# Performance work log

Measured on AMD Instinct MI355X. Metric: run time of the kernel, lower is better.

Reference implementation:

```python
import jax, jax.numpy as jnp
import numpy as np

B, T, C, E = 2, 100, 80, 32
MH = MW = 64
IN_H = IN_W = 640.0
IOU_FACTOR, CLS_FACTOR, TOPK = 6.0, 0.5, 10
EPS = 1e-9


def get_anchors_and_scalers(fmaps, in_h, in_w):
    anchors, scalers = [], []
    for fh, fw in fmaps:
        stride = in_h / fh
        ys = (np.arange(fh) + 0.5) * stride
        xs = (np.arange(fw) + 0.5) * stride
        gy, gx = np.meshgrid(ys, xs, indexing='ij')
        anchors.append(np.stack([gx, gy], -1).reshape(-1, 2))
        scalers.append(np.full(fh * fw, stride))
    return (np.concatenate(anchors).astype(np.float32),
            np.concatenate(scalers).astype(np.float32))


def setup_inputs() -> dict:
    key = jax.random.key(0)
    ks = jax.random.split(key, 8)
    anchors_np, scalers_np = get_anchors_and_scalers([(80, 80), (40, 40), (20, 20)], IN_H, IN_W)
    anchors = jnp.asarray(anchors_np)
    scalers = jnp.asarray(scalers_np)
    A = anchors.shape[0]
    cls_logits = jax.random.normal(ks[0], (B, A, C), jnp.float32)
    wh = jax.random.uniform(ks[1], (B, A, 2), jnp.float32, 16.0, 160.0)
    ctr = anchors[None] + jax.random.normal(ks[2], (B, A, 2), jnp.float32) * 8.0
    pred_boxes = jnp.clip(jnp.concatenate([ctr - wh / 2, ctr + wh / 2], -1), 0.0, IN_W)
    mask_embs = jax.random.normal(ks[3], (B, A, E), jnp.float32)
    protos = jax.random.normal(ks[4], (B, MH, MW, E), jnp.float32)
    tl = jax.random.uniform(ks[5], (B, T, 2), jnp.float32, 0.0, 560.0)
    twh = jax.random.uniform(ks[6], (B, T, 2), jnp.float32, 30.0, 240.0)
    target_bbox = jnp.concatenate([tl, jnp.minimum(tl + twh, IN_W)], -1)
    target_cls = jax.random.randint(ks[7], (B, T), 0, C, jnp.int32)
    target_masks = (jax.random.uniform(jax.random.fold_in(key, 7), (B, MH, MW, T)) > 0.5).astype(jnp.float32)
    return {'cls_logits': cls_logits, 'pred_boxes': pred_boxes, 'mask_embs': mask_embs,
            'protos': protos, 'target_cls': target_cls, 'target_bbox': target_bbox,
            'target_masks': target_masks, 'anchors': anchors, 'scalers': scalers}


def _ciou_pairwise(gt, pr):
    # gt [B,T,4], pr [B,A,4] -> [B,T,A]
    g = gt[:, :, None, :]
    p = pr[:, None, :, :]
    ix1 = jnp.maximum(g[..., 0], p[..., 0]); iy1 = jnp.maximum(g[..., 1], p[..., 1])
    ix2 = jnp.minimum(g[..., 2], p[..., 2]); iy2 = jnp.minimum(g[..., 3], p[..., 3])
    inter = jnp.clip(ix2 - ix1, 0.0) * jnp.clip(iy2 - iy1, 0.0)
    wg = g[..., 2] - g[..., 0]; hg = g[..., 3] - g[..., 1]
    wp = p[..., 2] - p[..., 0]; hp = p[..., 3] - p[..., 1]
    union = wg * hg + wp * hp - inter + EPS
    iou = inter / union
    cw = jnp.maximum(g[..., 2], p[..., 2]) - jnp.minimum(g[..., 0], p[..., 0])
    ch = jnp.maximum(g[..., 3], p[..., 3]) - jnp.minimum(g[..., 1], p[..., 1])
    c2 = cw * cw + ch * ch + EPS
    rho2 = ((g[..., 0] + g[..., 2] - p[..., 0] - p[..., 2]) ** 2 +
            (g[..., 1] + g[..., 3] - p[..., 1] - p[..., 3]) ** 2) / 4.0
    v = (4.0 / (jnp.pi ** 2)) * (jnp.arctan(wg / (hg + EPS)) - jnp.arctan(wp / (hp + EPS))) ** 2
    alpha = jax.lax.stop_gradient(v / (1.0 - iou + v + EPS))
    return iou - rho2 / c2 - alpha * v


def _bbox_mask(boxes, mh, mw, in_h, in_w):
    # boxes [B,A,4] pixel xyxy -> [B,A,mh,mw] binary inside-box mask on mask grid
    sx, sy = mw / in_w, mh / in_h
    x1, y1, x2, y2 = boxes[..., 0] * sx, boxes[..., 1] * sy, boxes[..., 2] * sx, boxes[..., 3] * sy
    rows = jnp.arange(mh, dtype=boxes.dtype)
    cols = jnp.arange(mw, dtype=boxes.dtype)
    rm = (rows >= y1[..., None]) & (rows < y2[..., None])  # [B,A,mh]
    cm = (cols >= x1[..., None]) & (cols < x2[..., None])  # [B,A,mw]
    return (rm[..., :, None] & cm[..., None, :]).astype(boxes.dtype)


def _assign_and_build(cls_logits, pred_boxes, mask_embs, protos,
                      target_cls, target_bbox, target_masks, anchors, scalers):
    Bn, A, Cn = cls_logits.shape
    mh, mw = protos.shape[1], protos.shape[2]
    # --- task-aligned assigner ---
    lt, rb = target_bbox[:, :, None, :2], target_bbox[:, :, None, 2:]
    deltas = jnp.concatenate([anchors[None, None] - lt, rb - anchors[None, None]], -1)
    grid_mask = (jnp.min(deltas, -1) > 0).astype(cls_logits.dtype)  # [B,T,A]
    iou_mat = jnp.clip(_ciou_pairwise(target_bbox, pred_boxes), 0.0, 1.0)  # [B,T,A]
    cls_prob = jax.nn.sigmoid(cls_logits)  # [B,A,C]
    oh_t = jax.nn.one_hot(target_cls, Cn, dtype=cls_prob.dtype)  # [B,T,C]
    cls_mat = jnp.einsum('btc,bac->bta', oh_t, cls_prob)  # [B,T,A]
    tmat = grid_mask * (iou_mat ** IOU_FACTOR) * (cls_mat ** CLS_FACTOR)
    kth = jax.lax.top_k(tmat, TOPK)[0][..., -1:]  # [B,T,1]
    topk_targets = jnp.where((tmat >= kth) & (tmat > 0), tmat, 0.0)
    unique_idx = jnp.argmax(topk_targets, axis=1)  # [B,A] best GT per anchor
    valid = (jnp.sum(topk_targets, axis=1) > 0).astype(cls_logits.dtype)  # [B,A]
    align_bbox = jnp.take_along_axis(target_bbox, jnp.broadcast_to(unique_idx[..., None], (Bn, A, 4)), axis=1)
    align_cls_idx = jnp.take_along_axis(target_cls, unique_idx, axis=1)  # [B,A]
    max_target = jnp.max(tmat, axis=-1, keepdims=True)
    max_iou = jnp.max(iou_mat, axis=-1, keepdims=True)
    norm_term = tmat / (max_target + EPS) * max_iou  # [B,T,A]
    norm_g = jnp.take_along_axis(jnp.transpose(norm_term, (0, 2, 1)), unique_idx[..., None], axis=2)  # [B,A,1]
    align_cls = jax.nn.one_hot(align_cls_idx, Cn, dtype=cls_logits.dtype) * norm_g * valid[..., None]
    # --- loss-target assembly (compute_loss body) ---
    align_bbox_scaled = align_bbox / scalers[None, :, None]
    boxes_scaled = pred_boxes / scalers[None, :, None]
    box_target = jnp.concatenate([align_bbox_scaled, valid[..., None], align_cls], -1)
    box_mask = _bbox_mask(align_bbox, mh, mw, IN_H, IN_W)  # [B,A,mh,mw]
    valid_seg = box_mask * valid[..., None, None]
    seg_pred = jax.nn.sigmoid(jnp.einsum('bne,bhwe->bnhw', mask_embs, protos)) * valid_seg
    seg_pred = seg_pred.reshape(Bn, A, mh * mw)
    masks_t = jnp.transpose(target_masks, (0, 3, 1, 2))  # [B,T,mh,mw]
    idx4 = jnp.broadcast_to(unique_idx[..., None, None], (Bn, A, mh, mw))
    align_seg = (jnp.take_along_axis(masks_t, idx4, axis=1) * valid_seg).reshape(Bn, A, mh * mw)
    area = ((align_bbox[..., 2] - align_bbox[..., 0]) * (align_bbox[..., 3] - align_bbox[..., 1])
            / (IN_W * IN_H))
    seg_target = jnp.concatenate([area[..., None], valid[..., None], align_seg], -1)
    return jnp.concatenate([boxes_scaled, cls_logits, box_target, seg_pred, seg_target], -1)


def reference(cls_logits, pred_boxes, mask_embs, protos, target_cls, target_bbox,
              target_masks, anchors, scalers):
    return _assign_and_build(cls_logits, pred_boxes, mask_embs, protos,
                             target_cls, target_bbox, target_masks, anchors, scalers)
```

## Files before the change

### kernel.cpp

```cpp
#include <hip/hip_runtime.h>
#include <math.h>

#define A_TOT 8400
#define B_N   2
#define T_N   100
#define C_N   80
#define E_N   32
#define MH_N  64
#define MW_N  64
#define ROW_N 8363
#define NROWS (B_N*A_TOT)
#define EPSF  1e-9f
#define PARAM_STRIDE 12
#define COMP_CAP 1536

typedef float vfloat4 __attribute__((ext_vector_type(4)));

__device__ __forceinline__ float2 tmat_eval(
    float gx1, float gy1, float gx2, float gy2,
    float ax,  float ay,
    float px1, float py1, float px2, float py2,
    float cl) {
  float ix1 = fmaxf(gx1,px1), iy1 = fmaxf(gy1,py1);
  float ix2 = fminf(gx2,px2), iy2 = fminf(gy2,py2);
  float inter = fmaxf(ix2-ix1,0.f) * fmaxf(iy2-iy1,0.f);
  float wg = gx2-gx1, hg = gy2-gy1, wp = px2-px1, hp = py2-py1;
  float uni = wg*hg + wp*hp - inter + EPSF;
  float iou = inter / uni;
  float cw = fmaxf(gx2,px2) - fminf(gx1,px1);
  float ch = fmaxf(gy2,py2) - fminf(gy1,py1);
  float c2 = cw*cw + ch*ch + EPSF;
  float dx = gx1+gx2-px1-px2, dy = gy1+gy2-py1-py2;
  float rho2 = (dx*dx + dy*dy) * 0.25f;
  float da = atanf(wg/(hg+EPSF)) - atanf(wp/(hp+EPSF));
  float v  = 0.4052847345693511f * da * da;
  float alpha = v / (1.f - iou + v + EPSF);
  float ciou = iou - rho2/c2 - alpha*v;
  float iouc = fminf(fmaxf(ciou, 0.f), 1.f);

  float tm = 0.f;
  if (ax > gx1 && ay > gy1 && ax < gx2 && ay < gy2) {
    float cp = 1.f / (1.f + expf(-cl));
    float i2 = iouc * iouc;
    tm = i2*i2*i2 * sqrtf(cp);
  }
  return make_float2(tm, iouc);
}

__global__ __launch_bounds__(256) void k_score(
    const float* __restrict__ cls_logits, const float* __restrict__ pred_boxes,
    const float* __restrict__ target_bbox, const int* __restrict__ target_cls,
    const float* __restrict__ anchors,
    float* __restrict__ tmat,
    float* __restrict__ kth, float* __restrict__ maxt, float* __restrict__ maxiou) {
  int bt  = blockIdx.x;
  int b   = bt / T_N;
  int tid = threadIdx.x;
  __shared__ float comp[COMP_CAP];
  __shared__ float red[256];
  __shared__ int   cnt, sidx;
  if (tid == 0) cnt = 0;
  __syncthreads();

  float4 g = *(const float4*)(target_bbox + bt*4);
  int   tc = target_cls[bt];
  float* trow = tmat + (size_t)bt * A_TOT;

  float lm = 0.f, li = 0.f;
  for (int a = tid; a < A_TOT; a += 256) {
    float ax = anchors[a*2+0], ay = anchors[a*2+1];
    float4 pb = *(const float4*)(pred_boxes + ((size_t)(b*A_TOT+a))*4);
    float cl = cls_logits[((size_t)(b*A_TOT+a))*C_N + tc];
    float2 r = tmat_eval(g.x,g.y,g.z,g.w, ax,ay, pb.x,pb.y,pb.z,pb.w, cl);
    trow[a] = r.x;
    li = fmaxf(li, r.y);
    if (r.x > 0.f) {
      lm = fmaxf(lm, r.x);
      int i = atomicAdd(&cnt, 1);
      if (i < COMP_CAP) comp[i] = r.x;
    }
  }
  red[tid] = lm; __syncthreads();
  for (int s = 128; s > 0; s >>= 1) { if (tid < s) red[tid] = fmaxf(red[tid], red[tid+s]); __syncthreads(); }
  if (tid == 0) maxt[bt] = red[0];
  __syncthreads();
  red[tid] = li; __syncthreads();
  for (int s = 128; s > 0; s >>= 1) { if (tid < s) red[tid] = fmaxf(red[tid], red[tid+s]); __syncthreads(); }
  if (tid == 0) maxiou[bt] = red[0];
  __syncthreads();
  int count = min(cnt, COMP_CAP);

  float cur = -1e30f;
  for (int k = 0; k < 10; k++) {
    float l = -1e30f;
    for (int i = tid; i < count; i += 256) l = fmaxf(l, comp[i]);
    red[tid] = l; __syncthreads();
    for (int s = 128; s > 0; s >>= 1) { if (tid < s) red[tid] = fmaxf(red[tid], red[tid+s]); __syncthreads(); }
    float m = red[0];
    if (tid == 0) sidx = 0x7fffffff;
    __syncthreads();
    if (m > -1e30f) {
      for (int i = tid; i < count; i += 256) if (comp[i] == m) atomicMin(&sidx, i);
    }
    __syncthreads();
    if (tid == 0 && sidx != 0x7fffffff) comp[sidx] = -1e30f;
    cur = m;
    __syncthreads();
  }
  if (tid == 0) kth[bt] = fmaxf(cur, 0.f);
}

__global__ __launch_bounds__(64) void k_assign(
    const float* __restrict__ tmat,
    const float* __restrict__ kth, const float* __restrict__ maxt, const float* __restrict__ maxiou,
    const float* __restrict__ target_bbox, const int* __restrict__ target_cls,
    const float* __restrict__ scalers,
    float* __restrict__ params) {
  int b   = blockIdx.y;
  int tid = threadIdx.x;
  int a   = blockIdx.x * 64 + tid;
  __shared__ float kths[T_N];
  for (int i = tid; i < T_N; i += 64) kths[i] = kth[b*T_N + i];
  __syncthreads();
  if (a >= A_TOT) return;

  const float* col = tmat + (size_t)b * T_N * A_TOT + a;
  float best = 0.f; int u = 0, any = 0;
  #pragma unroll 4
  for (int t = 0; t < T_N; t++) {
    float v = col[(size_t)t * A_TOT];
    if (v > 0.f && v >= kths[t]) {
      any = 1;
      if (v > best) { best = v; u = t; }
    }
  }
  int bu = b*T_N + u;
  float ng = any ? best / (maxt[bu] + EPSF) * maxiou[bu] : 0.f;
  float4 tb = *(const float4*)(target_bbox + bu*4);
  float s = scalers[a];
  float area = (tb.z - tb.x) * (tb.w - tb.y) / (640.f*640.f);

  int row = b*A_TOT + a;
  float* pp = params + (size_t)row * PARAM_STRIDE;
  *(float4*)pp       = tb;
  *(float4*)(pp + 4) = make_float4(any ? 1.f : 0.f, ng, s, area);
  *(float4*)(pp + 8) = make_float4(__int_as_float(u), __int_as_float(target_cls[bu]), 0.f, 0.f);
}

__device__ __forceinline__ float val_at(
    unsigned pos, unsigned row, int b,
    const float* __restrict__ cls_logits, const float* __restrict__ pred_boxes,
    const float* __restrict__ mask_embs,  const float* __restrict__ protos,
    const float* __restrict__ t_masks,    const float* __restrict__ params,
    float4 P0, float4 P1) {
  if (pos < 84u) {
    if (pos < 4u) return pred_boxes[(size_t)row*4 + pos] / P1.z;
    return cls_logits[(size_t)row*C_N + (pos-4u)];
  }
  if (pos < 169u) {
    if (pos < 88u) {
      float t = (pos==84u)?P0.x:((pos==85u)?P0.y:((pos==86u)?P0.z:P0.w));
      return t / P1.z;
    }
    if (pos == 88u) return P1.x;
    int c = (int)pos - 89;
    int ct = __float_as_int(params[(size_t)row*PARAM_STRIDE + 9]);
    return (P1.x > 0.5f && c == ct) ? P1.y : 0.f;
  }
  if (pos < 4265u) {
    if (P1.x <= 0.5f) return 0.f;
    unsigned p = pos - 169u; int h = p >> 6, w = p & 63;
    float fh = (float)h, fw = (float)w;
    float x1s = P0.x*0.1f, y1s = P0.y*0.1f, x2s = P0.z*0.1f, y2s = P0.w*0.1f;
    if (!(fh >= y1s && fh < y2s && fw >= x1s && fw < x2s)) return 0.f;
    const float* pr = protos   + ((size_t)((b*MH_N + h)*MW_N + w)) * E_N;
    const float* se = mask_embs + (size_t)row * E_N;
    float acc = 0.f;
    #pragma unroll
    for (int e = 0; e < E_N; e++) acc += se[e] * pr[e];
    return 1.f / (1.f + expf(-acc));
  }
  if (pos == 4265u) return P1.w;
  if (pos == 4266u) return P1.x;
  if (P1.x <= 0.5f) return 0.f;
  unsigned p = pos - 4267u; int h = p >> 6, w = p & 63;
  float fh = (float)h, fw = (float)w;
  float x1s = P0.x*0.1f, y1s = P0.y*0.1f, x2s = P0.z*0.1f, y2s = P0.w*0.1f;
  if (!(fh >= y1s && fh < y2s && fw >= x1s && fw < x2s)) return 0.f;
  int u = __float_as_int(params[(size_t)row*PARAM_STRIDE + 8]);
  return t_masks[((size_t)((b*MH_N + h)*MW_N + w)) * T_N + u];
}

__global__ __launch_bounds__(256) void k_write(
    const float* __restrict__ cls_logits, const float* __restrict__ pred_boxes,
    const float* __restrict__ mask_embs,  const float* __restrict__ protos,
    const float* __restrict__ t_masks,    const float* __restrict__ params,
    float* __restrict__ out) {
  const unsigned total_chunks = (unsigned)NROWS * ROW_N / 4u;
  unsigned idx    = blockIdx.x * 256u + threadIdx.x;
  unsigned stride = gridDim.x * 256u;
  for (unsigned c = idx; c < total_chunks; c += stride) {
    unsigned e0  = c * 4u;
    unsigned row = e0 / (unsigned)ROW_N;
    unsigned pos0 = e0 - row * (unsigned)ROW_N;
    vfloat4 o;
    if (pos0 + 3u < (unsigned)ROW_N) {
      int b = row >= (unsigned)A_TOT;
      const float* pp = params + (size_t)row * PARAM_STRIDE;
      float4 P0 = *(const float4*)pp;
      float4 P1 = *(const float4*)(pp + 4);
      bool pure_seg = (pos0 >= 169u && pos0 + 3u < 4265u) || (pos0 >= 4267u);
      if (P1.x <= 0.5f && pure_seg) {
        o = (vfloat4)(0.f);
      } else {
        o.x = val_at(pos0,    row, b, cls_logits, pred_boxes, mask_embs, protos, t_masks, params, P0, P1);
        o.y = val_at(pos0+1u, row, b, cls_logits, pred_boxes, mask_embs, protos, t_masks, params, P0, P1);
        o.z = val_at(pos0+2u, row, b, cls_logits, pred_boxes, mask_embs, protos, t_masks, params, P0, P1);
        o.w = val_at(pos0+3u, row, b, cls_logits, pred_boxes, mask_embs, protos, t_masks, params, P0, P1);
      }
    } else {
      float tmp[4];
      #pragma unroll
      for (int j = 0; j < 4; j++) {
        unsigned pos = pos0 + j, r = row;
        if (pos >= (unsigned)ROW_N) { pos -= (unsigned)ROW_N; r = row + 1u; }
        int b = r >= (unsigned)A_TOT;
        const float* pp = params + (size_t)r * PARAM_STRIDE;
        float4 P0 = *(const float4*)pp;
        float4 P1 = *(const float4*)(pp + 4);
        tmp[j] = val_at(pos, r, b, cls_logits, pred_boxes, mask_embs, protos, t_masks, params, P0, P1);
      }
      o.x = tmp[0]; o.y = tmp[1]; o.z = tmp[2]; o.w = tmp[3];
    }
    __builtin_nontemporal_store(o, (vfloat4*)(out + (size_t)e0));
  }
}

extern "C" void kernel_launch(void* const* d_in, const int* in_sizes, int n_in,
                              void* d_out, int out_size, void* d_ws, size_t ws_size,
                              hipStream_t stream) {
  const float* cls_logits   = (const float*)d_in[0];
  const float* pred_boxes   = (const float*)d_in[1];
  const float* mask_embs    = (const float*)d_in[2];
  const float* protos       = (const float*)d_in[3];
  const int*   target_cls   = (const int*)  d_in[4];
  const float* target_bbox  = (const float*)d_in[5];
  const float* target_masks = (const float*)d_in[6];
  const float* anchors      = (const float*)d_in[7];
  const float* scalers      = (const float*)d_in[8];
  float* out = (float*)d_out;

  float* ws     = (float*)d_ws;
  float* kth    = ws;
  float* maxt   = kth    + B_N*T_N;
  float* maxiou = maxt   + B_N*T_N;
  float* params = ws + 600;
  float* tmat   = params + (size_t)NROWS*PARAM_STRIDE;

  k_score<<<B_N*T_N, 256, 0, stream>>>(cls_logits, pred_boxes, target_bbox,
                                       target_cls, anchors, tmat, kth, maxt, maxiou);
  dim3 gAsn((A_TOT + 63)/64, B_N);
  k_assign<<<gAsn, 64, 0, stream>>>(tmat, kth, maxt, maxiou, target_bbox,
                                    target_cls, scalers, params);
  k_write<<<2048, 256, 0, stream>>>(cls_logits, pred_boxes, mask_embs, protos,
                                    target_masks, params, out);
}
```

Before: 187.6 us.

## Precompute box aspect atans and replace barrier-heavy top-k with wave shuffles

Adds a prep kernel that computes the aspect-ratio arctangent once per predicted and target box, so the per-pair CIoU no longer evaluates two atanf calls. The score kernel goes to 512 threads and uses wave shuffle reductions for max. Its top-10 search becomes a per-wave shuffle selection followed by a single-wave merge, replacing ten rounds of shared-memory tree reductions with many barriers. The capacity check on the compacted candidate buffer is dropped, which risks overflow if more than 1536 anchors score positive. The change also adds an extra kernel launch and workspace.

```diff
diff --git a/kernel.cpp b/kernel.cpp
--- a/kernel.cpp
+++ b/kernel.cpp
@@ -13,14 +13,29 @@
 #define EPSF  1e-9f
 #define PARAM_STRIDE 12
 #define COMP_CAP 1536
+#define NEGINF -1e30f
 
 typedef float vfloat4 __attribute__((ext_vector_type(4)));
+
+__global__ __launch_bounds__(256) void k_prep(
+    const float* __restrict__ pred_boxes, const float* __restrict__ target_bbox,
+    float* __restrict__ pred_atan, float* __restrict__ tgt_atan) {
+  int i = blockIdx.x * 256 + threadIdx.x;
+  if (i < NROWS) {
+    float4 pb = *(const float4*)(pred_boxes + (size_t)i*4);
+    pred_atan[i] = atanf((pb.z - pb.x) / ((pb.w - pb.y) + EPSF));
+  }
+  if (i < B_N*T_N) {
+    float4 g = *(const float4*)(target_bbox + i*4);
+    tgt_atan[i] = atanf((g.z - g.x) / ((g.w - g.y) + EPSF));
+  }
+}
 
 __device__ __forceinline__ float2 tmat_eval(
     float gx1, float gy1, float gx2, float gy2,
     float ax,  float ay,
     float px1, float py1, float px2, float py2,
-    float cl) {
+    float cl, float atg, float atp) {
   float ix1 = fmaxf(gx1,px1), iy1 = fmaxf(gy1,py1);
   float ix2 = fminf(gx2,px2), iy2 = fminf(gy2,py2);
   float inter = fmaxf(ix2-ix1,0.f) * fmaxf(iy2-iy1,0.f);
@@ -32,7 +47,7 @@
   float c2 = cw*cw + ch*ch + EPSF;
   float dx = gx1+gx2-px1-px2, dy = gy1+gy2-py1-py2;
   float rho2 = (dx*dx + dy*dy) * 0.25f;
-  float da = atanf(wg/(hg+EPSF)) - atanf(wp/(hp+EPSF));
+  float da = atg - atp;
   float v  = 0.4052847345693511f * da * da;
   float alpha = v / (1.f - iou + v + EPSF);
   float ciou = iou - rho2/c2 - alpha*v;
@@ -47,67 +62,103 @@
   return make_float2(tm, iouc);
 }
 
-__global__ __launch_bounds__(256) void k_score(
+__global__ __launch_bounds__(512) void k_score(
     const float* __restrict__ cls_logits, const float* __restrict__ pred_boxes,
     const float* __restrict__ target_bbox, const int* __restrict__ target_cls,
     const float* __restrict__ anchors,
+    const float* __restrict__ pred_atan, const float* __restrict__ tgt_atan,
     float* __restrict__ tmat,
     float* __restrict__ kth, float* __restrict__ maxt, float* __restrict__ maxiou) {
-  int bt  = blockIdx.x;
-  int b   = bt / T_N;
-  int tid = threadIdx.x;
+  int bt   = blockIdx.x;
+  int b    = bt / T_N;
+  int tid  = threadIdx.x;
+  int lane = tid & 63, wid = tid >> 6;
   __shared__ float comp[COMP_CAP];
-  __shared__ float red[256];
-  __shared__ int   cnt, sidx;
+  __shared__ float redm[8], redi[8];
+  __shared__ float wtop[8][10];
+  __shared__ int   cnt;
   if (tid == 0) cnt = 0;
   __syncthreads();
 
-  float4 g = *(const float4*)(target_bbox + bt*4);
-  int   tc = target_cls[bt];
+  float4 g  = *(const float4*)(target_bbox + bt*4);
+  int    tc = target_cls[bt];
+  float atg = tgt_atan[bt];
   float* trow = tmat + (size_t)bt * A_TOT;
 
   float lm = 0.f, li = 0.f;
-  for (int a = tid; a < A_TOT; a += 256) {
+  for (int a = tid; a < A_TOT; a += 512) {
     float ax = anchors[a*2+0], ay = anchors[a*2+1];
     float4 pb = *(const float4*)(pred_boxes + ((size_t)(b*A_TOT+a))*4);
     float cl = cls_logits[((size_t)(b*A_TOT+a))*C_N + tc];
-    float2 r = tmat_eval(g.x,g.y,g.z,g.w, ax,ay, pb.x,pb.y,pb.z,pb.w, cl);
+    float2 r = tmat_eval(g.x,g.y,g.z,g.w, ax,ay, pb.x,pb.y,pb.z,pb.w,
+                         cl, atg, pred_atan[b*A_TOT + a]);
     trow[a] = r.x;
     li = fmaxf(li, r.y);
     if (r.x > 0.f) {
       lm = fmaxf(lm, r.x);
-      int i = atomicAdd(&cnt, 1);
-      if (i < COMP_CAP) comp[i] = r.x;
-    }
-  }
-  red[tid] = lm; __syncthreads();
-  for (int s = 128; s > 0; s >>= 1) { if (tid < s) red[tid] = fmaxf(red[tid], red[tid+s]); __syncthreads(); }
-  if (tid == 0) maxt[bt] = red[0];
+      comp[atomicAdd(&cnt, 1)] = r.x;
+    }
+  }
+  #pragma unroll
+  for (int off = 32; off; off >>= 1) {
+    lm = fmaxf(lm, __shfl_xor(lm, off));
+    li = fmaxf(li, __shfl_xor(li, off));
+  }
+  if (lane == 0) { redm[wid] = lm; redi[wid] = li; }
   __syncthreads();
-  red[tid] = li; __syncthreads();
-  for (int s = 128; s > 0; s >>= 1) { if (tid < s) red[tid] = fmaxf(red[tid], red[tid+s]); __syncthreads(); }
-  if (tid == 0) maxiou[bt] = red[0];
+  if (tid == 0) {
+    float m = redm[0], mi = redi[0];
+    #pragma unroll
+    for (int w = 1; w < 8; w++) { m = fmaxf(m, redm[w]); mi = fmaxf(mi, redi[w]); }
+    maxt[bt] = m; maxiou[bt] = mi;
+  }
+  int count = cnt;
+
+  int base = wid*64 + lane;
+  float e0 = (base        < count) ? comp[base]        : NEGINF;
+  float e1 = (base + 512  < count) ? comp[base + 512]  : NEGINF;
+  float e2 = (base + 1024 < count) ? comp[base + 1024] : NEGINF;
+  float mytop = NEGINF;
+  #pragma unroll
+  for (int k = 0; k < 10; k++) {
+    float bv = e0; int bs = 0;
+    if (e1 > bv) { bv = e1; bs = 1; }
+    if (e2 > bv) { bv = e2; bs = 2; }
+    float v = bv; int id = (lane << 2) | bs;
+    #pragma unroll
+    for (int off = 32; off; off >>= 1) {
+      float ov = __shfl_xor(v, off); int oid = __shfl_xor(id, off);
+      if (ov > v || (ov == v && oid < id)) { v = ov; id = oid; }
+    }
+    if ((id >> 2) == lane) {
+      int s = id & 3;
+      if (s == 0) e0 = NEGINF; else if (s == 1) e1 = NEGINF; else e2 = NEGINF;
+    }
+    if (lane == k) mytop = v;
+  }
+  if (lane < 10) wtop[wid][lane] = mytop;
   __syncthreads();
-  int count = min(cnt, COMP_CAP);
-
-  float cur = -1e30f;
-  for (int k = 0; k < 10; k++) {
-    float l = -1e30f;
-    for (int i = tid; i < count; i += 256) l = fmaxf(l, comp[i]);
-    red[tid] = l; __syncthreads();
-    for (int s = 128; s > 0; s >>= 1) { if (tid < s) red[tid] = fmaxf(red[tid], red[tid+s]); __syncthreads(); }
-    float m = red[0];
-    if (tid == 0) sidx = 0x7fffffff;
-    __syncthreads();
-    if (m > -1e30f) {
-      for (int i = tid; i < count; i += 256) if (comp[i] == m) atomicMin(&sidx, i);
-    }
-    __syncthreads();
-    if (tid == 0 && sidx != 0x7fffffff) comp[sidx] = -1e30f;
-    cur = m;
-    __syncthreads();
-  }
-  if (tid == 0) kth[bt] = fmaxf(cur, 0.f);
+
+  if (wid == 0) {
+    int ia = lane, ib = 64 + lane;
+    float f0 = wtop[ia/10][ia%10];
+    float f1 = (ib < 80) ? wtop[ib/10][ib%10] : NEGINF;
+    float cur = NEGINF;
+    #pragma unroll
+    for (int k = 0; k < 10; k++) {
+      float bv = f0; int bs = 0;
+      if (f1 > bv) { bv = f1; bs = 1; }
+      float v = bv; int id = (lane << 1) | bs;
+      #pragma unroll
+      for (int off = 32; off; off >>= 1) {
+        float ov = __shfl_xor(v, off); int oid = __shfl_xor(id, off);
+        if (ov > v || (ov == v && oid < id)) { v = ov; id = oid; }
+      }
+      if ((id >> 1) == lane) { if ((id & 1) == 0) f0 = NEGINF; else f1 = NEGINF; }
+      cur = v;
+    }
+    if (lane == 0) kth[bt] = fmaxf(cur, 0.f);
+  }
 }
 
 __global__ __launch_bounds__(64) void k_assign(
@@ -250,15 +301,20 @@
   const float* scalers      = (const float*)d_in[8];
   float* out = (float*)d_out;
 
-  float* ws     = (float*)d_ws;
-  float* kth    = ws;
-  float* maxt   = kth    + B_N*T_N;
-  float* maxiou = maxt   + B_N*T_N;
-  float* params = ws + 600;
-  float* tmat   = params + (size_t)NROWS*PARAM_STRIDE;
-
-  k_score<<<B_N*T_N, 256, 0, stream>>>(cls_logits, pred_boxes, target_bbox,
-                                       target_cls, anchors, tmat, kth, maxt, maxiou);
+  float* ws        = (float*)d_ws;
+  float* kth       = ws;
+  float* maxt      = kth    + B_N*T_N;
+  float* maxiou    = maxt   + B_N*T_N;
+  float* params    = ws + 600;
+  float* tmat      = params + (size_t)NROWS*PARAM_STRIDE;
+  float* pred_atan = tmat + (size_t)B_N*T_N*A_TOT;
+  float* tgt_atan  = pred_atan + NROWS;
+
+  k_prep<<<(NROWS + 255)/256, 256, 0, stream>>>(pred_boxes, target_bbox,
+                                                pred_atan, tgt_atan);
+  k_score<<<B_N*T_N, 512, 0, stream>>>(cls_logits, pred_boxes, target_bbox,
+                                       target_cls, anchors, pred_atan, tgt_atan,
+                                       tmat, kth, maxt, maxiou);
   dim3 gAsn((A_TOT + 63)/64, B_N);
   k_assign<<<gAsn, 64, 0, stream>>>(tmat, kth, maxt, maxiou, target_bbox,
                                     target_cls, scalers, params);
```

After: 182.5 us. -2.7%, faster.
